# Performance work log

Hardware: AMD Instinct MI355X
Metric: run time of the kernel (lower is better)

The kernel has to match this reference:

```python
import jax, jax.numpy as jnp
import numpy as np

ALPHA = 0.2
BN_EPS = 1e-5
NEG = -9e15


def make_quaternion_mul(kernel):
    # kernel: [in/4, out]; split columns into quaternion components
    dim = kernel.shape[1] // 4
    r, i, j, k = jnp.split(kernel, 4, axis=1)
    r2 = jnp.concatenate([r, -i, -j, -k], axis=0)
    i2 = jnp.concatenate([i, r, -k, j], axis=0)
    j2 = jnp.concatenate([j, k, r, -i], axis=0)
    k2 = jnp.concatenate([k, -j, i, r], axis=0)
    return jnp.concatenate([r2, i2, j2, k2], axis=1)  # [in, out]


def setup_inputs() -> dict:
    key = jax.random.key(0)
    k1, k2, k3, k4 = jax.random.split(key, 4)
    N, IN, OUT = 8192, 512, 128
    inp = jax.random.normal(k1, (N, IN), dtype=jnp.float32)
    adj = jax.random.randint(k2, (N, N), 0, 2, dtype=jnp.int32)
    # xavier-like init for params
    W = jax.random.normal(k3, (IN // 4, OUT), dtype=jnp.float32) * (1.0 / np.sqrt(IN // 4))
    a = jax.random.normal(k4, (2 * OUT, 1), dtype=jnp.float32) * (1.0 / np.sqrt(2 * OUT))
    bn_gamma = jnp.ones((OUT,), dtype=jnp.float32)
    bn_beta = jnp.zeros((OUT,), dtype=jnp.float32)
    return {"input": inp, "adj": adj, "W": W, "a": a, "bn_gamma": bn_gamma, "bn_beta": bn_beta}


def reference(input, adj, W, a, bn_gamma, bn_beta):
    out_features = W.shape[1]
    hamilton = make_quaternion_mul(W)           # [in, out]
    h = input @ hamilton                        # [N, out]
    # a_input[i,j] = concat(h_i, h_j); a_input @ a decomposes as
    # (h @ a1)_i + (h @ a2)_j with a1 = a[:out], a2 = a[out:]
    a1 = a[:out_features, 0]                    # [out]
    a2 = a[out_features:, 0]                    # [out]
    s1 = h @ a1                                 # [N]
    s2 = h @ a2                                 # [N]
    e = s1[:, None] + s2[None, :]               # [N, N]
    e = jnp.where(e > 0, e, ALPHA * e)          # leaky_relu
    attention = jnp.where(adj > 0, e, NEG)
    attention = jax.nn.softmax(attention, axis=1)
    # dropout is identity in inference
    h_prime = attention @ h                     # [N, out]
    # BatchNorm1d (training-mode batch statistics, biased variance)
    mean = jnp.mean(h_prime, axis=0)
    var = jnp.var(h_prime, axis=0)
    h_prime = (h_prime - mean) / jnp.sqrt(var + BN_EPS) * bn_gamma + bn_beta
    # concat=True -> ELU
    return jax.nn.elu(h_prime)
```

## Files before the change

### kernel.cpp

```cpp
#include <hip/hip_runtime.h>
#include <hip/hip_bf16.h>
#include <math.h>

#define N_NODES 8192
#define IN_F    512
#define OUT_F   128
#define LRELU_A 0.2f
#define EPS_BN  1e-5f
#define MSH     40.0f
#define NSPLIT  8
#define JSPAN   (N_NODES / NSPLIT)
#define TILE_I  64
#define CH      64
#define HSTR    72

typedef unsigned short u16;
typedef unsigned int   u32;
typedef __attribute__((ext_vector_type(8))) short  short8;
typedef __attribute__((ext_vector_type(4))) float  floatx4;

__device__ __forceinline__ u16 f2bf_rtn(float x) {
    u32 u = __float_as_uint(x);
    return (u16)((u + 0x7fffu + ((u >> 16) & 1u)) >> 16);
}

__global__ __launch_bounds__(256) void k_h(const float* __restrict__ inp, const float* __restrict__ W,
                                           const float* __restrict__ a,
                                           u16* __restrict__ hT, float* __restrict__ s1, float* __restrict__ s2,
                                           float* __restrict__ cs, float* __restrict__ cq) {
    __shared__ float s1b[16], s2b[16];
    const int t = threadIdx.x;
    if (t < 16) { s1b[t] = 0.f; s2b[t] = 0.f; }
    if (blockIdx.x == 0 && t < OUT_F) { cs[t] = 0.f; cq[t] = 0.f; }
    __syncthreads();
    const int rg = t >> 4, cg = t & 15;
    const int r = blockIdx.x * 16 + rg;
    const int b = cg >> 2, cc0 = (cg & 3) * 8;
    const u32 NEGMASK = 0x284Eu;
    float acc[8];
#pragma unroll
    for (int q = 0; q < 8; q++) acc[q] = 0.f;
    const float* row = inp + (size_t)r * IN_F;
    for (int k8 = 0; k8 < IN_F; k8 += 8) {
        const int p = k8 >> 7;
        const float sg = (NEGMASK >> (b * 4 + p)) & 1u ? -1.f : 1.f;
        const float* wbase = W + (b ^ p) * 32 + cc0;
        float4 x0 = *(const float4*)(row + k8);
        float4 x1 = *(const float4*)(row + k8 + 4);
        float xv[8] = {x0.x, x0.y, x0.z, x0.w, x1.x, x1.y, x1.z, x1.w};
#pragma unroll
        for (int dk = 0; dk < 8; dk++) {
            const int q = (k8 + dk) & 127;
            const float* wp = wbase + q * 128;
            float4 w0 = *(const float4*)wp;
            float4 w1 = *(const float4*)(wp + 4);
            const float av = xv[dk] * sg;
            acc[0] += av * w0.x; acc[1] += av * w0.y; acc[2] += av * w0.z; acc[3] += av * w0.w;
            acc[4] += av * w1.x; acc[5] += av * w1.y; acc[6] += av * w1.z; acc[7] += av * w1.w;
        }
    }
    float s1p = 0.f, s2p = 0.f;
#pragma unroll
    for (int q = 0; q < 8; q++) {
        const int c = (cg << 3) + q;
        hT[(size_t)c * N_NODES + r] = f2bf_rtn(acc[q]);
        s1p += acc[q] * a[c];
        s2p += acc[q] * a[OUT_F + c];
    }
    atomicAdd(&s1b[rg], s1p);
    atomicAdd(&s2b[rg], s2p);
    __syncthreads();
    if (t < 16) { s1[blockIdx.x * 16 + t] = s1b[t]; s2[blockIdx.x * 16 + t] = s2b[t]; }
}

__global__ __launch_bounds__(256) void k_att(const int* __restrict__ adj, const u16* __restrict__ hT,
                                             const float* __restrict__ s1, const float* __restrict__ s2,
                                             float* __restrict__ Opart, float* __restrict__ Lpart) {
    __shared__ u16 hs[2][128 * HSTR];
    __shared__ float s2s[JSPAN];
    const int t = threadIdx.x;
    const int lane = t & 63, wid = t >> 6;
    const int quad = lane >> 4, n = lane & 15;
    const int i0 = blockIdx.x * TILE_I;
    const int jbase = blockIdx.y * JSPAN;
    const int i_lane = i0 + wid * 16 + n;
    const float s1v = s1[i_lane];
    const int c_st = t >> 1, jh = (t & 1) * 32;

    *(float4*)&s2s[t * 4] = *(const float4*)&s2[jbase + t * 4];

    floatx4 acc[8];
#pragma unroll
    for (int ct = 0; ct < 8; ct++) acc[ct] = (floatx4){0.f, 0.f, 0.f, 0.f};
    float Lacc = 0.f;

    const int* adjp = adj + (size_t)i_lane * N_NODES;
    const u16* hTp = hT + (size_t)c_st * N_NODES + jh;

    uint4 A0 = *(const uint4*)(adjp + jbase + quad * 8);
    uint4 A1 = *(const uint4*)(adjp + jbase + quad * 8 + 4);
    uint4 A2 = *(const uint4*)(adjp + jbase + 32 + quad * 8);
    uint4 A3 = *(const uint4*)(adjp + jbase + 32 + quad * 8 + 4);
    {
        const u16* ph = hTp + jbase;
        *(uint4*)&hs[0][c_st * HSTR + jh]      = *(const uint4*)(ph);
        *(uint4*)&hs[0][c_st * HSTR + jh + 8]  = *(const uint4*)(ph + 8);
        *(uint4*)&hs[0][c_st * HSTR + jh + 16] = *(const uint4*)(ph + 16);
        *(uint4*)&hs[0][c_st * HSTR + jh + 24] = *(const uint4*)(ph + 24);
    }
    __syncthreads();

    const int nch = JSPAN / CH;
    for (int k = 0; k < nch; k++) {
        const int cur = k & 1, nxt = cur ^ 1;
        const bool more = (k + 1 < nch);
        const int j1 = more ? (jbase + (k + 1) * CH) : jbase;
        uint4 N0 = *(const uint4*)(adjp + j1 + quad * 8);
        uint4 N1 = *(const uint4*)(adjp + j1 + quad * 8 + 4);
        uint4 N2 = *(const uint4*)(adjp + j1 + 32 + quad * 8);
        uint4 N3 = *(const uint4*)(adjp + j1 + 32 + quad * 8 + 4);
        const u16* ph = hTp + j1;
        uint4 H0 = *(const uint4*)(ph);
        uint4 H1 = *(const uint4*)(ph + 8);
        uint4 H2 = *(const uint4*)(ph + 16);
        uint4 H3 = *(const uint4*)(ph + 24);

        const u32 av[16] = {A0.x, A0.y, A0.z, A0.w, A1.x, A1.y, A1.z, A1.w,
                            A2.x, A2.y, A2.z, A2.w, A3.x, A3.y, A3.z, A3.w};
        short8 fa0, fa1;
        const int sbase = k * CH + quad * 8;
#pragma unroll
        for (int jj = 0; jj < 8; jj++) {
            float sc0 = s1v + s2s[sbase + jj];
            float sc1 = s1v + s2s[sbase + 32 + jj];
            sc0 = fmaxf(sc0, LRELU_A * sc0);
            sc1 = fmaxf(sc1, LRELU_A * sc1);
            float w0 = ((int)av[jj] > 0)     ? __expf(sc0 - MSH) : 0.f;
            float w1 = ((int)av[8 + jj] > 0) ? __expf(sc1 - MSH) : 0.f;
            Lacc += w0; Lacc += w1;
            fa0[jj] = (short)f2bf_rtn(w0);
            fa1[jj] = (short)f2bf_rtn(w1);
        }
#pragma unroll
        for (int ct = 0; ct < 8; ct++) {
            const int boff = (ct * 16 + n) * HSTR + quad * 8;
            short8 fb0 = *(const short8*)&hs[cur][boff];
            short8 fb1 = *(const short8*)&hs[cur][boff + 32];
            acc[ct] = __builtin_amdgcn_mfma_f32_16x16x32_bf16(fa0, fb0, acc[ct], 0, 0, 0);
            acc[ct] = __builtin_amdgcn_mfma_f32_16x16x32_bf16(fa1, fb1, acc[ct], 0, 0, 0);
        }
        if (more) {
            *(uint4*)&hs[nxt][c_st * HSTR + jh]      = H0;
            *(uint4*)&hs[nxt][c_st * HSTR + jh + 8]  = H1;
            *(uint4*)&hs[nxt][c_st * HSTR + jh + 16] = H2;
            *(uint4*)&hs[nxt][c_st * HSTR + jh + 24] = H3;
        }
        __syncthreads();
        A0 = N0; A1 = N1; A2 = N2; A3 = N3;
    }

    Lacc += __shfl_xor(Lacc, 16, 64);
    Lacc += __shfl_xor(Lacc, 32, 64);
    if (lane < 16)
        Lpart[(size_t)blockIdx.y * N_NODES + i_lane] = Lacc;

    const size_t obase = (size_t)blockIdx.y * N_NODES * OUT_F;
#pragma unroll
    for (int ct = 0; ct < 8; ct++) {
#pragma unroll
        for (int r = 0; r < 4; r++) {
            const int i = i0 + wid * 16 + quad * 4 + r;
            Opart[obase + (size_t)i * OUT_F + ct * 16 + n] = acc[ct][r];
        }
    }
}

__global__ __launch_bounds__(256) void k_comb(const float* __restrict__ Opart, const float* __restrict__ Lpart,
                                              float* __restrict__ hp, float* __restrict__ cs, float* __restrict__ cq) {
    const int t = threadIdx.x;
    const int c = t & 127, half = t >> 7;
    const int ibase = blockIdx.x * 16;
    float sv = 0.f, sq = 0.f;
    for (int k = 0; k < 8; k++) {
        const int i = ibase + half + (k << 1);
        float o = 0.f, L = 0.f;
#pragma unroll
        for (int s = 0; s < NSPLIT; s++) {
            o += Opart[((size_t)s * N_NODES + i) * OUT_F + c];
            L += Lpart[(size_t)s * N_NODES + i];
        }
        float v = L > 0.f ? o / L : 0.f;
        hp[(size_t)i * OUT_F + c] = v;
        sv += v; sq += v * v;
    }
    __shared__ float red[256];
    red[t] = sv; __syncthreads();
    if (half == 0) atomicAdd(&cs[c], sv + red[t + 128]);
    __syncthreads(); red[t] = sq; __syncthreads();
    if (half == 0) atomicAdd(&cq[c], sq + red[t + 128]);
}

__global__ __launch_bounds__(256) void k_bn(const float* __restrict__ hp, const float* __restrict__ cs,
                                            const float* __restrict__ cq, const float* __restrict__ gamma,
                                            const float* __restrict__ beta, float* __restrict__ out) {
    const int idx = blockIdx.x * 256 + threadIdx.x;
    const int c = idx & 127;
    const float mean = cs[c] * (1.f / N_NODES);
    const float var  = cq[c] * (1.f / N_NODES) - mean * mean;
    float x = (hp[idx] - mean) * rsqrtf(var + EPS_BN) * gamma[c] + beta[c];
    x = x > 0.f ? x : expm1f(x);
    out[idx] = x;
}

extern "C" void kernel_launch(void* const* d_in, const int* in_sizes, int n_in,
                              void* d_out, int out_size, void* d_ws, size_t ws_size,
                              hipStream_t stream) {
    (void)in_sizes; (void)n_in; (void)out_size; (void)ws_size;
    const float* inp   = (const float*)d_in[0];
    const int*   adj   = (const int*)d_in[1];
    const float* W     = (const float*)d_in[2];
    const float* a     = (const float*)d_in[3];
    const float* gamma = (const float*)d_in[4];
    const float* beta  = (const float*)d_in[5];
    float* out = (float*)d_out;

    char* wsb = (char*)d_ws;
    u16*   hT  = (u16*)wsb;    wsb += (size_t)OUT_F * N_NODES * 2;
    float* s1  = (float*)wsb;  wsb += N_NODES * 4;
    float* s2  = (float*)wsb;  wsb += N_NODES * 4;
    float* Op  = (float*)wsb;  wsb += (size_t)NSPLIT * N_NODES * OUT_F * 4;
    float* Lp  = (float*)wsb;  wsb += (size_t)NSPLIT * N_NODES * 4;
    float* hp  = (float*)wsb;  wsb += (size_t)N_NODES * OUT_F * 4;
    float* cs  = (float*)wsb;  wsb += OUT_F * 4;
    float* cq  = (float*)wsb;  wsb += OUT_F * 4;

    hipLaunchKernelGGL(k_h,    dim3(512), dim3(256), 0, stream, inp, W, a, hT, s1, s2, cs, cq);
    hipLaunchKernelGGL(k_att,  dim3(128, NSPLIT), dim3(256), 0, stream, adj, hT, s1, s2, Op, Lp);
    hipLaunchKernelGGL(k_comb, dim3(512), dim3(256), 0, stream, Op, Lp, hp, cs, cq);
    hipLaunchKernelGGL(k_bn,   dim3(4096), dim3(256), 0, stream, hp, cs, cq, gamma, beta, out);
}
```

Measured before the change: 519.9 us.

## Stage full per-block h slice in LDS once and drop per-chunk barriers

Doubles the j-split so each block covers 512 columns and loads the whole 128x512 bf16 h slice into shared memory up front, removing the double-buffered chunk loop and its per-iteration __syncthreads. Adjacency prefetch now goes through a register ring of 128-column chunks, and the s2 values are read with vector loads. This removes barrier stalls and gives the MFMA loop more independent work per chunk. In exchange, shared memory per block grows to about 130KB, which limits occupancy to one block per CU, and twice as many partial outputs must be written and reduced.

After: 540.6 us. 4.0% more time.

```diff
diff --git a/kernel.cpp b/kernel.cpp
--- a/kernel.cpp
+++ b/kernel.cpp
@@ -8,11 +8,11 @@
 #define LRELU_A 0.2f
 #define EPS_BN  1e-5f
 #define MSH     40.0f
-#define NSPLIT  8
+#define NSPLIT  16
 #define JSPAN   (N_NODES / NSPLIT)
 #define TILE_I  64
-#define CH      64
-#define HSTR    72
+#define CH      128
+#define HSTR    520
 
 typedef unsigned short u16;
 typedef unsigned int   u32;
@@ -76,7 +76,7 @@
 __global__ __launch_bounds__(256) void k_att(const int* __restrict__ adj, const u16* __restrict__ hT,
                                              const float* __restrict__ s1, const float* __restrict__ s2,
                                              float* __restrict__ Opart, float* __restrict__ Lpart) {
-    __shared__ u16 hs[2][128 * HSTR];
+    __shared__ u16 hs[128 * HSTR];
     __shared__ float s2s[JSPAN];
     const int t = threadIdx.x;
     const int lane = t & 63, wid = t >> 6;
@@ -85,78 +85,70 @@
     const int jbase = blockIdx.y * JSPAN;
     const int i_lane = i0 + wid * 16 + n;
     const float s1v = s1[i_lane];
-    const int c_st = t >> 1, jh = (t & 1) * 32;
-
-    *(float4*)&s2s[t * 4] = *(const float4*)&s2[jbase + t * 4];
+
+    if (t < 128) *(float4*)&s2s[t * 4] = *(const float4*)&s2[jbase + t * 4];
+    {
+        const int cr = t >> 1, off = (t & 1) * 256;
+        const u16* src = hT + (size_t)cr * N_NODES + jbase + off;
+        u16* dst = &hs[cr * HSTR + off];
+#pragma unroll
+        for (int v = 0; v < 32; v++)
+            *(uint4*)(dst + v * 8) = *(const uint4*)(src + v * 8);
+    }
 
     floatx4 acc[8];
 #pragma unroll
     for (int ct = 0; ct < 8; ct++) acc[ct] = (floatx4){0.f, 0.f, 0.f, 0.f};
     float Lacc = 0.f;
 
-    const int* adjp = adj + (size_t)i_lane * N_NODES;
-    const u16* hTp = hT + (size_t)c_st * N_NODES + jh;
-
-    uint4 A0 = *(const uint4*)(adjp + jbase + quad * 8);
-    uint4 A1 = *(const uint4*)(adjp + jbase + quad * 8 + 4);
-    uint4 A2 = *(const uint4*)(adjp + jbase + 32 + quad * 8);
-    uint4 A3 = *(const uint4*)(adjp + jbase + 32 + quad * 8 + 4);
-    {
-        const u16* ph = hTp + jbase;
-        *(uint4*)&hs[0][c_st * HSTR + jh]      = *(const uint4*)(ph);
-        *(uint4*)&hs[0][c_st * HSTR + jh + 8]  = *(const uint4*)(ph + 8);
-        *(uint4*)&hs[0][c_st * HSTR + jh + 16] = *(const uint4*)(ph + 16);
-        *(uint4*)&hs[0][c_st * HSTR + jh + 24] = *(const uint4*)(ph + 24);
+    const int* adjp = adj + (size_t)i_lane * N_NODES + jbase;
+    uint4 P[8];
+#pragma unroll
+    for (int ks = 0; ks < 4; ks++) {
+        P[2 * ks]     = *(const uint4*)(adjp + ks * 32 + quad * 8);
+        P[2 * ks + 1] = *(const uint4*)(adjp + ks * 32 + quad * 8 + 4);
     }
     __syncthreads();
 
-    const int nch = JSPAN / CH;
-    for (int k = 0; k < nch; k++) {
-        const int cur = k & 1, nxt = cur ^ 1;
-        const bool more = (k + 1 < nch);
-        const int j1 = more ? (jbase + (k + 1) * CH) : jbase;
-        uint4 N0 = *(const uint4*)(adjp + j1 + quad * 8);
-        uint4 N1 = *(const uint4*)(adjp + j1 + quad * 8 + 4);
-        uint4 N2 = *(const uint4*)(adjp + j1 + 32 + quad * 8);
-        uint4 N3 = *(const uint4*)(adjp + j1 + 32 + quad * 8 + 4);
-        const u16* ph = hTp + j1;
-        uint4 H0 = *(const uint4*)(ph);
-        uint4 H1 = *(const uint4*)(ph + 8);
-        uint4 H2 = *(const uint4*)(ph + 16);
-        uint4 H3 = *(const uint4*)(ph + 24);
-
-        const u32 av[16] = {A0.x, A0.y, A0.z, A0.w, A1.x, A1.y, A1.z, A1.w,
-                            A2.x, A2.y, A2.z, A2.w, A3.x, A3.y, A3.z, A3.w};
-        short8 fa0, fa1;
-        const int sbase = k * CH + quad * 8;
-#pragma unroll
-        for (int jj = 0; jj < 8; jj++) {
-            float sc0 = s1v + s2s[sbase + jj];
-            float sc1 = s1v + s2s[sbase + 32 + jj];
-            sc0 = fmaxf(sc0, LRELU_A * sc0);
-            sc1 = fmaxf(sc1, LRELU_A * sc1);
-            float w0 = ((int)av[jj] > 0)     ? __expf(sc0 - MSH) : 0.f;
-            float w1 = ((int)av[8 + jj] > 0) ? __expf(sc1 - MSH) : 0.f;
-            Lacc += w0; Lacc += w1;
-            fa0[jj] = (short)f2bf_rtn(w0);
-            fa1[jj] = (short)f2bf_rtn(w1);
-        }
-#pragma unroll
-        for (int ct = 0; ct < 8; ct++) {
-            const int boff = (ct * 16 + n) * HSTR + quad * 8;
-            short8 fb0 = *(const short8*)&hs[cur][boff];
-            short8 fb1 = *(const short8*)&hs[cur][boff + 32];
-            acc[ct] = __builtin_amdgcn_mfma_f32_16x16x32_bf16(fa0, fb0, acc[ct], 0, 0, 0);
-            acc[ct] = __builtin_amdgcn_mfma_f32_16x16x32_bf16(fa1, fb1, acc[ct], 0, 0, 0);
-        }
-        if (more) {
-            *(uint4*)&hs[nxt][c_st * HSTR + jh]      = H0;
-            *(uint4*)&hs[nxt][c_st * HSTR + jh + 8]  = H1;
-            *(uint4*)&hs[nxt][c_st * HSTR + jh + 16] = H2;
-            *(uint4*)&hs[nxt][c_st * HSTR + jh + 24] = H3;
-        }
-        __syncthreads();
-        A0 = N0; A1 = N1; A2 = N2; A3 = N3;
+#pragma unroll
+    for (int k = 0; k < JSPAN / CH; k++) {
+        uint4 C[8];
+#pragma unroll
+        for (int v = 0; v < 8; v++) C[v] = P[v];
+        if (k + 1 < JSPAN / CH) {
+            const int* ap = adjp + (k + 1) * CH;
+#pragma unroll
+            for (int ks = 0; ks < 4; ks++) {
+                P[2 * ks]     = *(const uint4*)(ap + ks * 32 + quad * 8);
+                P[2 * ks + 1] = *(const uint4*)(ap + ks * 32 + quad * 8 + 4);
+            }
+        }
+        short8 fa[4];
+#pragma unroll
+        for (int ks = 0; ks < 4; ks++) {
+            const int jl = k * CH + ks * 32 + quad * 8;
+            float4 sa = *(const float4*)&s2s[jl];
+            float4 sb = *(const float4*)&s2s[jl + 4];
+            const float sv[8] = {sa.x, sa.y, sa.z, sa.w, sb.x, sb.y, sb.z, sb.w};
+            const u32 am[8] = {C[2*ks].x, C[2*ks].y, C[2*ks].z, C[2*ks].w,
+                               C[2*ks+1].x, C[2*ks+1].y, C[2*ks+1].z, C[2*ks+1].w};
+#pragma unroll
+            for (int jj = 0; jj < 8; jj++) {
+                float sc = s1v + sv[jj];
+                sc = fmaxf(sc, LRELU_A * sc);
+                float w = ((int)am[jj] > 0) ? __expf(sc - MSH) : 0.f;
+                Lacc += w;
+                fa[ks][jj] = (short)f2bf_rtn(w);
+            }
+        }
+#pragma unroll
+        for (int ks = 0; ks < 4; ks++) {
+#pragma unroll
+            for (int ct = 0; ct < 8; ct++) {
+                short8 fb = *(const short8*)&hs[(ct * 16 + n) * HSTR + k * CH + ks * 32 + quad * 8];
+                acc[ct] = __builtin_amdgcn_mfma_f32_16x16x32_bf16(fa[ks], fb, acc[ct], 0, 0, 0);
+            }
+        }
     }
 
     Lacc += __shfl_xor(Lacc, 16, 64);
```
